# Optimization experiments

Hardware: AMD Instinct MI355X
Metric: run time of the kernel (lower is better)

The kernel has to match this reference:

```python
import jax, jax.numpy as jnp
import numpy as np

N, IN, OUT, T = 65536, 256, 256, 8


def setup_inputs() -> dict:
    key = jax.random.key(0)
    k1, k2, k3, k4 = jax.random.split(key, 4)
    x = jax.random.normal(k1, (N, IN), dtype=jnp.float32)
    types = jax.random.randint(k2, (N,), 0, T, dtype=jnp.int32)
    # xavier_uniform for W: limit = sqrt(6 / (fan_in + fan_out)) with fan computed
    # on the last two dims (out_size, in_size)
    limit = float(np.sqrt(6.0 / (IN + OUT)))
    W = jax.random.uniform(k3, (T, OUT, IN), dtype=jnp.float32, minval=-limit, maxval=limit)
    # original inits b to zeros; use small random values so the bias path is exercised
    b = 0.01 * jax.random.normal(k4, (T, OUT), dtype=jnp.float32)
    return {"x": x, "types": types, "W": W, "b": b}


def reference(x, types, W, b):
    # out[i] = W[types[i]] @ x[i] + b[types[i]]
    # Grouped-GEMM expressed as a loop over the small fixed set of types,
    # avoiding the huge [N, OUT, IN] gather of W[types].
    num_types = W.shape[0]
    out = b[types]  # [N, OUT]
    for t in range(num_types):
        mask = (types == t)[:, None]  # [N, 1]
        out = out + jnp.where(mask, x @ W[t].T, jnp.float32(0.0))
    return out
```

## Files before the change

kernel.cpp:

```cpp
#include <hip/hip_runtime.h>
#include <stdint.h>


#define NROWS 65536
#define NTYPES 8
#define KDIM 256
#define ODIM 256
#define BM 64
#define MAX_TILES (NROWS / BM + NTYPES - 1)

typedef __attribute__((ext_vector_type(8))) short short8;
typedef __attribute__((ext_vector_type(4))) float f32x4;

__device__ __forceinline__ unsigned short f2bf(float f) {
    unsigned int u = __float_as_uint(f);
    u += 0x7fffu + ((u >> 16) & 1u);
    return (unsigned short)(u >> 16);
}

__global__ void prep_bucket_kernel(const float* __restrict__ W,
                                   unsigned short* __restrict__ Wp,
                                   const int* __restrict__ types,
                                   int* __restrict__ cnt,
                                   int* __restrict__ idx) {
    const int b = blockIdx.x;
    if (b < 256) {
        const int gid = b * 256 + threadIdx.x;
        const int t = gid >> 13;
        const int rem = gid & 8191;
        const int f = rem >> 9;
        const int q = (rem >> 6) & 7;
        const int l = rem & 63;
        const float* src = W + ((size_t)t * ODIM + f * 16 + (l & 15)) * KDIM
                             + q * 32 + (l >> 4) * 8;
        const float4 v0 = *(const float4*)src;
        const float4 v1 = *(const float4*)(src + 4);
        ushort4 p0, p1;
        p0.x = f2bf(v0.x); p0.y = f2bf(v0.y); p0.z = f2bf(v0.z); p0.w = f2bf(v0.w);
        p1.x = f2bf(v1.x); p1.y = f2bf(v1.y); p1.z = f2bf(v1.z); p1.w = f2bf(v1.w);
        ushort4* dst = (ushort4*)(Wp + (size_t)gid * 8);
        dst[0] = p0; dst[1] = p1;
    } else {
        __shared__ int h[NTYPES];
        __shared__ int base[NTYPES];
        int i = (b - 256) * 256 + threadIdx.x;
        if (threadIdx.x < NTYPES) h[threadIdx.x] = 0;
        __syncthreads();
        int t = types[i];
        int r = atomicAdd(&h[t], 1);
        __syncthreads();
        if (threadIdx.x < NTYPES)
            base[threadIdx.x] = atomicAdd(&cnt[threadIdx.x], h[threadIdx.x]);
        __syncthreads();
        idx[t * NROWS + base[t] + r] = i;
    }
}

__global__ __launch_bounds__(256, 4)
void gemm_kernel(const float* __restrict__ x,
                 const float* __restrict__ bias,
                 const unsigned short* __restrict__ Wp,
                 const int* __restrict__ cnt,
                 const int* __restrict__ idx,
                 float* __restrict__ out) {
    const int bid = blockIdx.x;
    int t = -1, m0 = 0, count = 0, accum = 0;
    #pragma unroll
    for (int i = 0; i < NTYPES; ++i) {
        int c = cnt[i];
        int ntile = (c + BM - 1) / BM;
        if (t < 0 && bid < accum + ntile) { t = i; m0 = (bid - accum) * BM; count = c; }
        accum += ntile;
    }
    if (t < 0) return;

    __shared__ unsigned short As[BM * KDIM];
    char* AsB = (char*)As;

    const int tid = threadIdx.x;
    const int srow = tid >> 4;
    const int sc   = tid & 15;

    #pragma unroll
    for (int p = 0; p < 4; ++p) {
        const int row = p * 16 + srow;
        const int gr = m0 + row;
        const int xr = idx[t * NROWS + (gr < count ? gr : count - 1)];
        const float* xs = x + (size_t)xr * KDIM;
        #pragma unroll
        for (int s = 0; s < 4; ++s) {
            const int slot = s * 16 + sc;
            const float4 v = *(const float4*)(xs + slot * 4);
            ushort4 pk;
            pk.x = f2bf(v.x); pk.y = f2bf(v.y); pk.z = f2bf(v.z); pk.w = f2bf(v.w);
            const int c = slot >> 1;
            *(ushort4*)(AsB + row * 512 + (c ^ (row & 7)) * 16 + (slot & 1) * 8) = pk;
        }
    }
    __syncthreads();

    const int wave = tid >> 6;
    const int lane = tid & 63;
    const int lr = lane & 15;
    const int lq = lane >> 4;

    const unsigned short* Wpt = Wp + (size_t)t * 16 * 8 * 512;

    f32x4 acc[4][4] = {};

    #pragma unroll
    for (int q = 0; q < 8; ++q) {
        short8 bf[4], af[4];
        #pragma unroll
        for (int j = 0; j < 4; ++j)
            bf[j] = *(const short8*)(Wpt + ((size_t)((wave * 4 + j) * 8 + q)) * 512
                                         + lane * 8);
        #pragma unroll
        for (int i = 0; i < 4; ++i) {
            const int row = i * 16 + lr;
            af[i] = *(const short8*)(AsB + row * 512
                                         + (((q << 2) + lq) ^ (row & 7)) * 16);
        }
        #pragma unroll
        for (int i = 0; i < 4; ++i)
            #pragma unroll
            for (int j = 0; j < 4; ++j)
                acc[i][j] = __builtin_amdgcn_mfma_f32_16x16x32_bf16(
                    af[i], bf[j], acc[i][j], 0, 0, 0);
    }

    float bv[4];
    #pragma unroll
    for (int j = 0; j < 4; ++j)
        bv[j] = bias[t * ODIM + wave * 64 + j * 16 + lr];

    #pragma unroll
    for (int i = 0; i < 4; ++i) {
        #pragma unroll
        for (int r = 0; r < 4; ++r) {
            const int lm = i * 16 + lq * 4 + r;
            const int gr = m0 + lm;
            if (gr < count) {
                const size_t orow = (size_t)idx[t * NROWS + gr] * ODIM;
                #pragma unroll
                for (int j = 0; j < 4; ++j)
                    out[orow + wave * 64 + j * 16 + lr] = acc[i][j][r] + bv[j];
            }
        }
    }
}

extern "C" void kernel_launch(void* const* d_in, const int* in_sizes, int n_in,
                              void* d_out, int out_size, void* d_ws, size_t ws_size,
                              hipStream_t stream) {
    const float* x     = (const float*)d_in[0];
    const int*   types = (const int*)d_in[1];
    const float* W     = (const float*)d_in[2];
    const float* b     = (const float*)d_in[3];
    float* out = (float*)d_out;

    char* ws = (char*)d_ws;
    int* cnt = (int*)ws;
    int* idx = (int*)(ws + 1024);
    unsigned short* Wp = (unsigned short*)(ws + 1024 + (size_t)NTYPES * NROWS * sizeof(int));

    hipMemsetAsync(cnt, 0, NTYPES * sizeof(int), stream);
    prep_bucket_kernel<<<512, 256, 0, stream>>>(W, Wp, types, cnt, idx);
    gemm_kernel<<<MAX_TILES, 256, 0, stream>>>(x, b, Wp, cnt, idx, out);
}
```

Before: 134.5 us.

## Halve gemm row tile, cache row indices in LDS, coalesce W prep reads

```diff
diff --git a/kernel.cpp b/kernel.cpp
--- a/kernel.cpp
+++ b/kernel.cpp
@@ -6,8 +6,8 @@
 #define NTYPES 8
 #define KDIM 256
 #define ODIM 256
-#define BM 64
-#define MAX_TILES (NROWS / BM + NTYPES - 1)
+#define BM 32
+#define MAX_TILES (NROWS / BM + NTYPES)
 
 typedef __attribute__((ext_vector_type(8))) short short8;
 typedef __attribute__((ext_vector_type(4))) float f32x4;
@@ -26,19 +26,21 @@
     const int b = blockIdx.x;
     if (b < 256) {
         const int gid = b * 256 + threadIdx.x;
-        const int t = gid >> 13;
-        const int rem = gid & 8191;
-        const int f = rem >> 9;
-        const int q = (rem >> 6) & 7;
-        const int l = rem & 63;
-        const float* src = W + ((size_t)t * ODIM + f * 16 + (l & 15)) * KDIM
-                             + q * 32 + (l >> 4) * 8;
+        const int R   = gid >> 5;
+        const int c32 = gid & 31;
+        const int t  = R >> 8;
+        const int r  = R & 255;
+        const int f  = r >> 4;
+        const int rr = r & 15;
+        const int q  = c32 >> 2;
+        const int l  = (c32 & 3) * 16 + rr;
+        const float* src = W + (size_t)R * KDIM + c32 * 8;
         const float4 v0 = *(const float4*)src;
         const float4 v1 = *(const float4*)(src + 4);
         ushort4 p0, p1;
         p0.x = f2bf(v0.x); p0.y = f2bf(v0.y); p0.z = f2bf(v0.z); p0.w = f2bf(v0.w);
         p1.x = f2bf(v1.x); p1.y = f2bf(v1.y); p1.z = f2bf(v1.z); p1.w = f2bf(v1.w);
-        ushort4* dst = (ushort4*)(Wp + (size_t)gid * 8);
+        ushort4* dst = (ushort4*)(Wp + (size_t)(((t * 16 + f) * 8 + q) * 512 + l * 8));
         dst[0] = p0; dst[1] = p1;
     } else {
         __shared__ int h[NTYPES];
@@ -56,7 +58,7 @@
     }
 }
 
-__global__ __launch_bounds__(256, 4)
+__global__ __launch_bounds__(256, 5)
 void gemm_kernel(const float* __restrict__ x,
                  const float* __restrict__ bias,
                  const unsigned short* __restrict__ Wp,
@@ -75,26 +77,30 @@
     if (t < 0) return;
 
     __shared__ unsigned short As[BM * KDIM];
+    __shared__ int idx_s[BM];
     char* AsB = (char*)As;
 
     const int tid = threadIdx.x;
-    const int srow = tid >> 4;
-    const int sc   = tid & 15;
+    const int srow = tid >> 3;
+    const int sc   = tid & 7;
 
-    #pragma unroll
-    for (int p = 0; p < 4; ++p) {
-        const int row = p * 16 + srow;
-        const int gr = m0 + row;
+    {
+        const int gr = m0 + srow;
         const int xr = idx[t * NROWS + (gr < count ? gr : count - 1)];
+        if (sc == 0) idx_s[srow] = xr;
         const float* xs = x + (size_t)xr * KDIM;
+        float4 av[8];
         #pragma unroll
-        for (int s = 0; s < 4; ++s) {
-            const int slot = s * 16 + sc;
-            const float4 v = *(const float4*)(xs + slot * 4);
+        for (int s = 0; s < 8; ++s)
+            av[s] = *(const float4*)(xs + (s * 8 + sc) * 4);
+        #pragma unroll
+        for (int s = 0; s < 8; ++s) {
+            const int slot = s * 8 + sc;
             ushort4 pk;
-            pk.x = f2bf(v.x); pk.y = f2bf(v.y); pk.z = f2bf(v.z); pk.w = f2bf(v.w);
+            pk.x = f2bf(av[s].x); pk.y = f2bf(av[s].y);
+            pk.z = f2bf(av[s].z); pk.w = f2bf(av[s].w);
             const int c = slot >> 1;
-            *(ushort4*)(AsB + row * 512 + (c ^ (row & 7)) * 16 + (slot & 1) * 8) = pk;
+            *(ushort4*)(AsB + srow * 512 + ((c ^ (srow & 7)) * 16) + (slot & 1) * 8) = pk;
         }
     }
     __syncthreads();
@@ -106,23 +112,23 @@
 
     const unsigned short* Wpt = Wp + (size_t)t * 16 * 8 * 512;
 
-    f32x4 acc[4][4] = {};
+    f32x4 acc[2][4] = {};
 
     #pragma unroll
     for (int q = 0; q < 8; ++q) {
-        short8 bf[4], af[4];
+        short8 bf[4], af[2];
         #pragma unroll
         for (int j = 0; j < 4; ++j)
             bf[j] = *(const short8*)(Wpt + ((size_t)((wave * 4 + j) * 8 + q)) * 512
                                          + lane * 8);
         #pragma unroll
-        for (int i = 0; i < 4; ++i) {
+        for (int i = 0; i < 2; ++i) {
             const int row = i * 16 + lr;
             af[i] = *(const short8*)(AsB + row * 512
                                          + (((q << 2) + lq) ^ (row & 7)) * 16);
         }
         #pragma unroll
-        for (int i = 0; i < 4; ++i)
+        for (int i = 0; i < 2; ++i)
             #pragma unroll
             for (int j = 0; j < 4; ++j)
                 acc[i][j] = __builtin_amdgcn_mfma_f32_16x16x32_bf16(
@@ -135,16 +141,18 @@
         bv[j] = bias[t * ODIM + wave * 64 + j * 16 + lr];
 
     #pragma unroll
-    for (int i = 0; i < 4; ++i) {
+    for (int i = 0; i < 2; ++i) {
         #pragma unroll
         for (int r = 0; r < 4; ++r) {
             const int lm = i * 16 + lq * 4 + r;
             const int gr = m0 + lm;
             if (gr < count) {
-                const size_t orow = (size_t)idx[t * NROWS + gr] * ODIM;
+                const size_t orow = (size_t)idx_s[lm] * ODIM;
                 #pragma unroll
                 for (int j = 0; j < 4; ++j)
-                    out[orow + wave * 64 + j * 16 + lr] = acc[i][j][r] + bv[j];
+                    __builtin_nontemporal_store(
+                        acc[i][j][r] + bv[j],
+                        &out[orow + wave * 64 + j * 16 + lr]);
             }
         }
     }
```

New measurement: 135.3 us. No clear change (+0.6%).

## Permute packed W columns to enable float4 output stores and cache row indices

Applied to the files above, without the earlier changes.

```diff
diff --git a/kernel.cpp b/kernel.cpp
--- a/kernel.cpp
+++ b/kernel.cpp
@@ -26,19 +26,21 @@
     const int b = blockIdx.x;
     if (b < 256) {
         const int gid = b * 256 + threadIdx.x;
-        const int t = gid >> 13;
-        const int rem = gid & 8191;
-        const int f = rem >> 9;
-        const int q = (rem >> 6) & 7;
-        const int l = rem & 63;
-        const float* src = W + ((size_t)t * ODIM + f * 16 + (l & 15)) * KDIM
-                             + q * 32 + (l >> 4) * 8;
+        const int R   = gid >> 5;
+        const int c32 = gid & 31;
+        const int t  = R >> 8;
+        const int r  = R & 255;
+        const int f  = r & 15;
+        const int rr = r >> 4;
+        const int q  = c32 >> 2;
+        const int l  = (c32 & 3) * 16 + rr;
+        const float* src = W + (size_t)R * KDIM + c32 * 8;
         const float4 v0 = *(const float4*)src;
         const float4 v1 = *(const float4*)(src + 4);
         ushort4 p0, p1;
         p0.x = f2bf(v0.x); p0.y = f2bf(v0.y); p0.z = f2bf(v0.z); p0.w = f2bf(v0.w);
         p1.x = f2bf(v1.x); p1.y = f2bf(v1.y); p1.z = f2bf(v1.z); p1.w = f2bf(v1.w);
-        ushort4* dst = (ushort4*)(Wp + (size_t)gid * 8);
+        ushort4* dst = (ushort4*)(Wp + (size_t)(((t * 16 + f) * 8 + q) * 512 + l * 8));
         dst[0] = p0; dst[1] = p1;
     } else {
         __shared__ int h[NTYPES];
@@ -75,9 +77,17 @@
     if (t < 0) return;
 
     __shared__ unsigned short As[BM * KDIM];
+    __shared__ int idx_s[BM];
     char* AsB = (char*)As;
 
     const int tid = threadIdx.x;
+    const int wave = tid >> 6;
+    const int lane = tid & 63;
+    const int lr = lane & 15;
+    const int lq = lane >> 4;
+
+    const float4 bv = *(const float4*)(bias + t * ODIM + lr * 16 + wave * 4);
+
     const int srow = tid >> 4;
     const int sc   = tid & 15;
 
@@ -86,6 +96,7 @@
         const int row = p * 16 + srow;
         const int gr = m0 + row;
         const int xr = idx[t * NROWS + (gr < count ? gr : count - 1)];
+        if (sc == 0) idx_s[row] = xr;
         const float* xs = x + (size_t)xr * KDIM;
         #pragma unroll
         for (int s = 0; s < 4; ++s) {
@@ -98,11 +109,6 @@
         }
     }
     __syncthreads();
-
-    const int wave = tid >> 6;
-    const int lane = tid & 63;
-    const int lr = lane & 15;
-    const int lq = lane >> 4;
 
     const unsigned short* Wpt = Wp + (size_t)t * 16 * 8 * 512;
 
@@ -129,11 +135,6 @@
                     af[i], bf[j], acc[i][j], 0, 0, 0);
     }
 
-    float bv[4];
-    #pragma unroll
-    for (int j = 0; j < 4; ++j)
-        bv[j] = bias[t * ODIM + wave * 64 + j * 16 + lr];
-
     #pragma unroll
     for (int i = 0; i < 4; ++i) {
         #pragma unroll
@@ -141,10 +142,13 @@
             const int lm = i * 16 + lq * 4 + r;
             const int gr = m0 + lm;
             if (gr < count) {
-                const size_t orow = (size_t)idx[t * NROWS + gr] * ODIM;
-                #pragma unroll
-                for (int j = 0; j < 4; ++j)
-                    out[orow + wave * 64 + j * 16 + lr] = acc[i][j][r] + bv[j];
+                const size_t orow = (size_t)idx_s[lm] * ODIM;
+                float4 v;
+                v.x = acc[i][0][r] + bv.x;
+                v.y = acc[i][1][r] + bv.y;
+                v.z = acc[i][2][r] + bv.z;
+                v.w = acc[i][3][r] + bv.w;
+                *(float4*)(out + orow + lr * 16 + wave * 4) = v;
             }
         }
     }
```

After: 146.1 us. 8.6% more time.
